# Kernel tuning notes

Measured on AMD Instinct MI355X. Metric: run time of the kernel, lower is better.

## Reference

```python
import jax, jax.numpy as jnp
import numpy as np

H, W = 4096, 4096
KH, KW = 16, 16


def setup_inputs() -> dict:
    key = jax.random.key(0)
    kx, kw = jax.random.split(key)
    x = jax.random.normal(kx, (H, W), dtype=jnp.float32)
    weight = jax.random.normal(kw, (KH, KW), dtype=jnp.float32)
    bias = jnp.zeros((1,), dtype=jnp.float32)
    return {"x": x, "weight": weight, "bias": bias}


def reference(x, weight, bias):
    # 2D valid cross-correlation (no kernel flip), single channel, + scalar bias.
    # lax.conv_general_dilated computes cross-correlation by default.
    lhs = x[None, None, :, :]          # [1,1,H,W]
    rhs = weight[None, None, :, :]     # [1,1,KH,KW]
    y = jax.lax.conv_general_dilated(
        lhs, rhs,
        window_strides=(1, 1),
        padding="VALID",
        dimension_numbers=("NCHW", "OIHW", "NCHW"),
    )[0, 0]                            # [H-KH+1, W-KW+1]
    return y + bias[0]
```

## Files before the change

### kernel.cpp

```cpp
#include <hip/hip_runtime.h>

#define IH 4096
#define IW 4096
#define KH 16
#define KW 16
#define OH 4081
#define OW 4081

#define TBR 64
#define TBC 128
#define LROWS 79
#define LSTR 192
#define BSTR 40

typedef short bf16x8 __attribute__((ext_vector_type(8)));
typedef float f32x4  __attribute__((ext_vector_type(4)));

static __device__ __forceinline__ unsigned int f2bf(float f) {
    unsigned int u = __float_as_uint(f);
    return (u + 0x7FFFu + ((u >> 16) & 1u)) >> 16;
}

__global__ void build_B(const float* __restrict__ wgt, unsigned short* __restrict__ Btab) {
    int idx = blockIdx.x * 256 + threadIdx.x;
    if (idx >= 16 * 16 * 32) return;
    int vp = idx & 31;
    int n  = (idx >> 5) & 15;
    int u  = idx >> 9;
    int t  = vp - n;
    float val = (t >= 0 && t < KW) ? wgt[u * KW + t] : 0.0f;
    Btab[idx] = (unsigned short)f2bf(val);
}

__global__ __launch_bounds__(512, 4)
void conv_mfma(const float* __restrict__ x,
               const unsigned short* __restrict__ Btab,
               const float* __restrict__ bias,
               float* __restrict__ out) {
    __shared__ unsigned short tile[LROWS * LSTR];
    __shared__ unsigned short ldsB[16 * 16 * BSTR];

    const int tid  = threadIdx.x;
    const int lane = tid & 63;
    const int wv   = tid >> 6;
    const int n    = lane & 15;
    const int q4   = lane >> 4;
    const int gy0  = blockIdx.y * TBR;
    const int gx0  = blockIdx.x * TBC;

    for (int idx = tid; idx < LROWS * 36; idx += 512) {
        int row = idx / 36;
        int c   = idx - row * 36;
        int gy  = gy0 + row;
        int gx  = gx0 + 4 * c;
        float4 q = make_float4(0.f, 0.f, 0.f, 0.f);
        if (gy < IH) {
            if (gx + 4 <= IW) {
                q = *reinterpret_cast<const float4*>(x + (size_t)gy * IW + gx);
            } else {
                float e0 = (gx + 0 < IW) ? x[(size_t)gy * IW + gx + 0] : 0.f;
                float e1 = (gx + 1 < IW) ? x[(size_t)gy * IW + gx + 1] : 0.f;
                float e2 = (gx + 2 < IW) ? x[(size_t)gy * IW + gx + 2] : 0.f;
                float e3 = (gx + 3 < IW) ? x[(size_t)gy * IW + gx + 3] : 0.f;
                q = make_float4(e0, e1, e2, e3);
            }
        }
        uint2 packed;
        packed.x = f2bf(q.x) | (f2bf(q.y) << 16);
        packed.y = f2bf(q.z) | (f2bf(q.w) << 16);
        int chunk = c >> 1;
        int half  = c & 1;
        int phys  = chunk ^ (row & 7);
        *reinterpret_cast<uint2*>(&tile[row * LSTR + phys * 8 + half * 4]) = packed;
    }

    for (int idx = tid; idx < 16 * 16 * 32; idx += 512) {
        int vp = idx & 31;
        int un = idx >> 5;
        ldsB[un * BSTR + vp] = Btab[idx];
    }
    __syncthreads();

    const int rb  = wv >> 1;
    const int cg  = wv & 1;
    const int li0 = rb * 16;

    f32x4 acc0 = {0.f, 0.f, 0.f, 0.f};
    f32x4 acc1 = {0.f, 0.f, 0.f, 0.f};
    f32x4 acc2 = {0.f, 0.f, 0.f, 0.f};
    f32x4 acc3 = {0.f, 0.f, 0.f, 0.f};

    const int cbase = cg * 8 + q4;

#pragma unroll
    for (int u = 0; u < KH; ++u) {
        bf16x8 bf = *reinterpret_cast<const bf16x8*>(&ldsB[(u * 16 + n) * BSTR + q4 * 8]);
        int row = li0 + n + u;
        int swz = row & 7;
        const unsigned short* rbase = &tile[row * LSTR];
        bf16x8 a0 = *reinterpret_cast<const bf16x8*>(rbase + ((cbase + 0) ^ swz) * 8);
        bf16x8 a1 = *reinterpret_cast<const bf16x8*>(rbase + ((cbase + 2) ^ swz) * 8);
        bf16x8 a2 = *reinterpret_cast<const bf16x8*>(rbase + ((cbase + 4) ^ swz) * 8);
        bf16x8 a3 = *reinterpret_cast<const bf16x8*>(rbase + ((cbase + 6) ^ swz) * 8);
        acc0 = __builtin_amdgcn_mfma_f32_16x16x32_bf16(a0, bf, acc0, 0, 0, 0);
        acc1 = __builtin_amdgcn_mfma_f32_16x16x32_bf16(a1, bf, acc1, 0, 0, 0);
        acc2 = __builtin_amdgcn_mfma_f32_16x16x32_bf16(a2, bf, acc2, 0, 0, 0);
        acc3 = __builtin_amdgcn_mfma_f32_16x16x32_bf16(a3, bf, acc3, 0, 0, 0);
    }

    const float bv = bias[0];
    const int orow0 = gy0 + li0 + q4 * 4;
    const int ocol0 = gx0 + cg * 64 + n;

#pragma unroll
    for (int t = 0; t < 4; ++t) {
        const f32x4 acc = (t == 0) ? acc0 : (t == 1) ? acc1 : (t == 2) ? acc2 : acc3;
        int col = ocol0 + t * 16;
        if (col < OW) {
#pragma unroll
            for (int r = 0; r < 4; ++r) {
                int rr = orow0 + r;
                if (rr < OH) out[(size_t)rr * OW + col] = acc[r] + bv;
            }
        }
    }
}

extern "C" void kernel_launch(void* const* d_in, const int* in_sizes, int n_in,
                              void* d_out, int out_size, void* d_ws, size_t ws_size,
                              hipStream_t stream) {
    const float* x  = (const float*)d_in[0];
    const float* w  = (const float*)d_in[1];
    const float* b  = (const float*)d_in[2];
    float* out = (float*)d_out;
    unsigned short* Btab = (unsigned short*)d_ws;

    build_B<<<32, 256, 0, stream>>>(w, Btab);

    dim3 grid((OW + TBC - 1) / TBC, (OH + TBR - 1) / TBR);
    conv_mfma<<<grid, dim3(512), 0, stream>>>(x, Btab, b, out);
}
```

Before: 135.5 us.

## Switch convolution to 32x32x16 MFMA with wider tiles and register-held Toeplitz B

Replaces the 16x16x32 MFMA formulation with 32x32x16 MFMAs. The block tile widens to 64x256 using 4 waves, and each wave reuses overlapping A fragments across four accumulators via a banded Toeplitz B. The B table is now read directly from global memory (L1/L2 cached) rather than staged through LDS. The LDS swizzle changes and the store path gets a fast unguarded branch for interior tiles. The aim is higher MFMA throughput per LDS read and fewer redundant tile loads, at the cost of higher register pressure and lower occupancy.

```diff
diff --git a/kernel.cpp b/kernel.cpp
--- a/kernel.cpp
+++ b/kernel.cpp
@@ -8,119 +8,126 @@
 #define OW 4081
 
 #define TBR 64
-#define TBC 128
+#define TBC 256
 #define LROWS 79
-#define LSTR 192
-#define BSTR 40
+#define LCH 40
+#define LSTR (LCH*8)
 
 typedef short bf16x8 __attribute__((ext_vector_type(8)));
-typedef float f32x4  __attribute__((ext_vector_type(4)));
+typedef float f32x16 __attribute__((ext_vector_type(16)));
 
 static __device__ __forceinline__ unsigned int f2bf(float f) {
     unsigned int u = __float_as_uint(f);
     return (u + 0x7FFFu + ((u >> 16) & 1u)) >> 16;
 }
 
-__global__ void build_B(const float* __restrict__ wgt, unsigned short* __restrict__ Btab) {
+__global__ void build_B(const float* __restrict__ wgt, unsigned short* __restrict__ Bt) {
     int idx = blockIdx.x * 256 + threadIdx.x;
-    if (idx >= 16 * 16 * 32) return;
-    int vp = idx & 31;
-    int n  = (idx >> 5) & 15;
-    int u  = idx >> 9;
+    if (idx >= 16 * 32 * 48) return;
+    int vp = idx % 48;
+    int n  = (idx / 48) & 31;
+    int u  = idx / (48 * 32);
     int t  = vp - n;
     float val = (t >= 0 && t < KW) ? wgt[u * KW + t] : 0.0f;
-    Btab[idx] = (unsigned short)f2bf(val);
+    Bt[idx] = (unsigned short)f2bf(val);
 }
 
-__global__ __launch_bounds__(512, 4)
-void conv_mfma(const float* __restrict__ x,
-               const unsigned short* __restrict__ Btab,
-               const float* __restrict__ bias,
-               float* __restrict__ out) {
+__global__ __launch_bounds__(256, 3)
+void conv_mfma32(const float* __restrict__ x,
+                 const unsigned short* __restrict__ Bt,
+                 const float* __restrict__ bias,
+                 float* __restrict__ out) {
     __shared__ unsigned short tile[LROWS * LSTR];
-    __shared__ unsigned short ldsB[16 * 16 * BSTR];
 
     const int tid  = threadIdx.x;
     const int lane = tid & 63;
     const int wv   = tid >> 6;
-    const int n    = lane & 15;
-    const int q4   = lane >> 4;
+    const int rb   = wv >> 1;
+    const int cb   = wv & 1;
+    const int m    = lane & 31;
+    const int hi   = lane >> 5;
     const int gy0  = blockIdx.y * TBR;
     const int gx0  = blockIdx.x * TBC;
 
-    for (int idx = tid; idx < LROWS * 36; idx += 512) {
-        int row = idx / 36;
-        int c   = idx - row * 36;
+    for (int idx = tid; idx < LROWS * 68; idx += 256) {
+        int row = idx / 68;
+        int c   = idx - row * 68;
         int gy  = gy0 + row;
         int gx  = gx0 + 4 * c;
         float4 q = make_float4(0.f, 0.f, 0.f, 0.f);
-        if (gy < IH) {
-            if (gx + 4 <= IW) {
-                q = *reinterpret_cast<const float4*>(x + (size_t)gy * IW + gx);
-            } else {
-                float e0 = (gx + 0 < IW) ? x[(size_t)gy * IW + gx + 0] : 0.f;
-                float e1 = (gx + 1 < IW) ? x[(size_t)gy * IW + gx + 1] : 0.f;
-                float e2 = (gx + 2 < IW) ? x[(size_t)gy * IW + gx + 2] : 0.f;
-                float e3 = (gx + 3 < IW) ? x[(size_t)gy * IW + gx + 3] : 0.f;
-                q = make_float4(e0, e1, e2, e3);
-            }
+        if (gy < IH && gx < IW) {
+            q = *reinterpret_cast<const float4*>(x + (size_t)gy * IW + gx);
         }
-        uint2 packed;
-        packed.x = f2bf(q.x) | (f2bf(q.y) << 16);
-        packed.y = f2bf(q.z) | (f2bf(q.w) << 16);
-        int chunk = c >> 1;
-        int half  = c & 1;
-        int phys  = chunk ^ (row & 7);
-        *reinterpret_cast<uint2*>(&tile[row * LSTR + phys * 8 + half * 4]) = packed;
-    }
-
-    for (int idx = tid; idx < 16 * 16 * 32; idx += 512) {
-        int vp = idx & 31;
-        int un = idx >> 5;
-        ldsB[un * BSTR + vp] = Btab[idx];
+        uint2 p;
+        p.x = f2bf(q.x) | (f2bf(q.y) << 16);
+        p.y = f2bf(q.z) | (f2bf(q.w) << 16);
+        int s    = (row ^ (row >> 3)) & 7;
+        int phys = (c >> 1) ^ s;
+        *reinterpret_cast<uint2*>(&tile[row * LSTR + phys * 8 + (c & 1) * 4]) = p;
     }
     __syncthreads();
 
-    const int rb  = wv >> 1;
-    const int cg  = wv & 1;
-    const int li0 = rb * 16;
+    f32x16 acc0 = {0,0,0,0,0,0,0,0,0,0,0,0,0,0,0,0};
+    f32x16 acc1 = {0,0,0,0,0,0,0,0,0,0,0,0,0,0,0,0};
+    f32x16 acc2 = {0,0,0,0,0,0,0,0,0,0,0,0,0,0,0,0};
+    f32x16 acc3 = {0,0,0,0,0,0,0,0,0,0,0,0,0,0,0,0};
 
-    f32x4 acc0 = {0.f, 0.f, 0.f, 0.f};
-    f32x4 acc1 = {0.f, 0.f, 0.f, 0.f};
-    f32x4 acc2 = {0.f, 0.f, 0.f, 0.f};
-    f32x4 acc3 = {0.f, 0.f, 0.f, 0.f};
-
-    const int cbase = cg * 8 + q4;
+    const int cB = cb * 16 + hi;
+    const unsigned short* Blane = Bt + m * 48 + hi * 8;
 
 #pragma unroll
     for (int u = 0; u < KH; ++u) {
-        bf16x8 bf = *reinterpret_cast<const bf16x8*>(&ldsB[(u * 16 + n) * BSTR + q4 * 8]);
-        int row = li0 + n + u;
-        int swz = row & 7;
-        const unsigned short* rbase = &tile[row * LSTR];
-        bf16x8 a0 = *reinterpret_cast<const bf16x8*>(rbase + ((cbase + 0) ^ swz) * 8);
-        bf16x8 a1 = *reinterpret_cast<const bf16x8*>(rbase + ((cbase + 2) ^ swz) * 8);
-        bf16x8 a2 = *reinterpret_cast<const bf16x8*>(rbase + ((cbase + 4) ^ swz) * 8);
-        bf16x8 a3 = *reinterpret_cast<const bf16x8*>(rbase + ((cbase + 6) ^ swz) * 8);
-        acc0 = __builtin_amdgcn_mfma_f32_16x16x32_bf16(a0, bf, acc0, 0, 0, 0);
-        acc1 = __builtin_amdgcn_mfma_f32_16x16x32_bf16(a1, bf, acc1, 0, 0, 0);
-        acc2 = __builtin_amdgcn_mfma_f32_16x16x32_bf16(a2, bf, acc2, 0, 0, 0);
-        acc3 = __builtin_amdgcn_mfma_f32_16x16x32_bf16(a3, bf, acc3, 0, 0, 0);
+        const int rowA = rb * 32 + m + u;
+        const int s    = (rowA ^ (rowA >> 3)) & 7;
+        const unsigned short* rbase = &tile[rowA * LSTR];
+
+        bf16x8 a[9];
+#pragma unroll
+        for (int d = 0; d < 9; ++d) {
+            int phys = (cB + 2 * d) ^ s;
+            a[d] = *reinterpret_cast<const bf16x8*>(rbase + phys * 8);
+        }
+        const unsigned short* Bu = Blane + u * (32 * 48);
+        bf16x8 b0 = *reinterpret_cast<const bf16x8*>(Bu + 0);
+        bf16x8 b1 = *reinterpret_cast<const bf16x8*>(Bu + 16);
+        bf16x8 b2 = *reinterpret_cast<const bf16x8*>(Bu + 32);
+
+        acc0 = __builtin_amdgcn_mfma_f32_32x32x16_bf16(a[0], b0, acc0, 0, 0, 0);
+        acc0 = __builtin_amdgcn_mfma_f32_32x32x16_bf16(a[1], b1, acc0, 0, 0, 0);
+        acc0 = __builtin_amdgcn_mfma_f32_32x32x16_bf16(a[2], b2, acc0, 0, 0, 0);
+        acc1 = __builtin_amdgcn_mfma_f32_32x32x16_bf16(a[2], b0, acc1, 0, 0, 0);
+        acc1 = __builtin_amdgcn_mfma_f32_32x32x16_bf16(a[3], b1, acc1, 0, 0, 0);
+        acc1 = __builtin_amdgcn_mfma_f32_32x32x16_bf16(a[4], b2, acc1, 0, 0, 0);
+        acc2 = __builtin_amdgcn_mfma_f32_32x32x16_bf16(a[4], b0, acc2, 0, 0, 0);
+        acc2 = __builtin_amdgcn_mfma_f32_32x32x16_bf16(a[5], b1, acc2, 0, 0, 0);
+        acc2 = __builtin_amdgcn_mfma_f32_32x32x16_bf16(a[6], b2, acc2, 0, 0, 0);
+        acc3 = __builtin_amdgcn_mfma_f32_32x32x16_bf16(a[6], b0, acc3, 0, 0, 0);
+        acc3 = __builtin_amdgcn_mfma_f32_32x32x16_bf16(a[7], b1, acc3, 0, 0, 0);
+        acc3 = __builtin_amdgcn_mfma_f32_32x32x16_bf16(a[8], b2, acc3, 0, 0, 0);
     }
 
-    const float bv = bias[0];
-    const int orow0 = gy0 + li0 + q4 * 4;
-    const int ocol0 = gx0 + cg * 64 + n;
+    const float bv   = bias[0];
+    const int   row0 = gy0 + rb * 32 + 4 * hi;
+    const int   col0 = gx0 + cb * 128 + m;
+    const bool  full = (gy0 + TBR <= OH) && (gx0 + TBC <= OW);
 
+    const f32x16* accs[4] = {&acc0, &acc1, &acc2, &acc3};
 #pragma unroll
-    for (int t = 0; t < 4; ++t) {
-        const f32x4 acc = (t == 0) ? acc0 : (t == 1) ? acc1 : (t == 2) ? acc2 : acc3;
-        int col = ocol0 + t * 16;
-        if (col < OW) {
+    for (int g = 0; g < 4; ++g) {
+        const f32x16 acc = *accs[g];
+        const int col = col0 + g * 32;
+        float* op = out + col;
+        if (full) {
 #pragma unroll
-            for (int r = 0; r < 4; ++r) {
-                int rr = orow0 + r;
-                if (rr < OH) out[(size_t)rr * OW + col] = acc[r] + bv;
+            for (int r = 0; r < 16; ++r) {
+                int rr = row0 + (r & 3) + 8 * (r >> 2);
+                op[(size_t)rr * OW] = acc[r] + bv;
+            }
+        } else if (col < OW) {
+#pragma unroll
+            for (int r = 0; r < 16; ++r) {
+                int rr = row0 + (r & 3) + 8 * (r >> 2);
+                if (rr < OH) op[(size_t)rr * OW] = acc[r] + bv;
             }
         }
     }
@@ -133,10 +140,10 @@
     const float* w  = (const float*)d_in[1];
     const float* b  = (const float*)d_in[2];
     float* out = (float*)d_out;
-    unsigned short* Btab = (unsigned short*)d_ws;
+    unsigned short* Bt = (unsigned short*)d_ws;
 
-    build_B<<<32, 256, 0, stream>>>(w, Btab);
+    build_B<<<96, 256, 0, stream>>>(w, Bt);
 
     dim3 grid((OW + TBC - 1) / TBC, (OH + TBR - 1) / TBR);
-    conv_mfma<<<grid, dim3(512), 0, stream>>>(x, Btab, b, out);
+    conv_mfma32<<<grid, dim3(256), 0, stream>>>(x, Bt, b, out);
 }
```

After: 153.2 us. 13.1% more time.
